# Kernel optimization log

Hardware: AMD Instinct MI355X
Metric: run time of the kernel (lower is better)

Reference implementation:

```python
import jax, jax.numpy as jnp
import numpy as np

LEAK = 0.95
THRESHOLD = 1.0
RESCALE = 2.0


def _xavier_uniform(key, shape, gain=2.0):
    fan_out, fan_in = shape
    bound = gain * np.sqrt(6.0 / (fan_in + fan_out))
    return jax.random.uniform(key, shape, jnp.float32, -bound, bound)


def setup_inputs() -> dict:
    key = jax.random.key(0)
    k_inp, k_w1, k_w2 = jax.random.split(key, 3)
    inp = jax.random.normal(k_inp, (8192, 784), jnp.float32)
    w1 = _xavier_uniform(k_w1, (800, 784))   # fc1.weight
    w2 = _xavier_uniform(k_w2, (10, 800))    # fc2.weight
    return {"inp": inp, "w1": w1, "w2": w2, "num_steps": 25}


@jax.custom_vjp
def spike_fn(x):
    return (x > 0).astype(x.dtype)

def _spike_fwd(x):
    return spike_fn(x), x

def _spike_bwd(x, g):
    # grad = g * 0.3 * relu(1 - |x|)  (surrogate BP)
    return (g * 0.3 * jnp.maximum(1.0 - jnp.abs(x), 0.0),)

spike_fn.defvjp(_spike_fwd, _spike_bwd)


def poisson_gen(key, inp):
    r = jax.random.uniform(key, inp.shape, inp.dtype)
    temp = (r * RESCALE <= jnp.abs(inp)).astype(inp.dtype) * jnp.sign(inp)
    return 0.5 * (temp + 1.0)


def reference(inp, w1, w2, num_steps):
    batch = inp.shape[0]
    x = inp.reshape(batch, -1)
    keys = jax.random.split(jax.random.key(42), num_steps)

    def step(carry, key):
        mem1, mem2 = carry
        sp = poisson_gen(key, x)                    # [B, 784]
        mem1 = LEAK * mem1 + (1.0 - LEAK) * (sp @ w1.T)  # [B, 800]
        mem_thr = mem1 / THRESHOLD - 1.0
        out = spike_fn(mem_thr)
        rst = jnp.where(mem_thr > 0, THRESHOLD, 0.0)
        mem1 = mem1 - jax.lax.stop_gradient(rst)
        mem2 = mem2 + out @ w2.T                    # [B, 10]
        return (mem1, mem2), None

    init = (jnp.zeros((batch, 800), x.dtype), jnp.zeros((batch, 10), x.dtype))
    (_, mem2), _ = jax.lax.scan(step, init, keys)
    return mem2 / num_steps
```

## Files before the change

### kernel.cpp

```cpp
#include <hip/hip_runtime.h>
#include <cstdint>

__host__ __device__ inline uint32_t tf_rotl32(uint32_t x, uint32_t r) {
  return (x << r) | (x >> (32u - r));
}

__host__ __device__ inline void threefry2x32(uint32_t k0, uint32_t k1,
                                             uint32_t x0, uint32_t x1,
                                             uint32_t* o0, uint32_t* o1) {
  uint32_t ks0 = k0, ks1 = k1, ks2 = k0 ^ k1 ^ 0x1BD11BDAu;
  x0 += ks0; x1 += ks1;
#define TF_R(r) { x0 += x1; x1 = tf_rotl32(x1, r); x1 ^= x0; }
  TF_R(13) TF_R(15) TF_R(26) TF_R(6)
  x0 += ks1; x1 += ks2 + 1u;
  TF_R(17) TF_R(29) TF_R(16) TF_R(24)
  x0 += ks2; x1 += ks0 + 2u;
  TF_R(13) TF_R(15) TF_R(26) TF_R(6)
  x0 += ks0; x1 += ks1 + 3u;
  TF_R(17) TF_R(29) TF_R(16) TF_R(24)
  x0 += ks1; x1 += ks2 + 4u;
  TF_R(13) TF_R(15) TF_R(26) TF_R(6)
  x0 += ks2; x1 += ks0 + 5u;
#undef TF_R
  *o0 = x0; *o1 = x1;
}

#define BSZ   8192
#define KIN   784
#define HID   800
#define NOUT  10
#define NSTEP 25


__global__ __launch_bounds__(256) void enc_kernel(const float* __restrict__ inp,
                                                  uint8_t* __restrict__ enc,
                                                  uint32_t k0, uint32_t k1) {
  int j = blockIdx.x * blockDim.x + threadIdx.x;
  if (j >= BSZ * KIN) return;
  uint32_t o0, o1;
  threefry2x32(k0, k1, 0u, (uint32_t)j, &o0, &o1);
  uint32_t bits = o0 ^ o1;
  float r = __uint_as_float((bits >> 9) | 0x3f800000u) - 1.0f;
  float x = inp[j];
  bool cond = (2.0f * r <= fabsf(x));
  int s = (x > 0.0f) ? 1 : ((x < 0.0f) ? -1 : 0);
  enc[j] = (uint8_t)(1 + (cond ? s : 0));
}

__global__ __launch_bounds__(256) void transpose_kernel(const float* __restrict__ w1,
                                                        float* __restrict__ w1t) {
  int idx = blockIdx.x * blockDim.x + threadIdx.x;
  if (idx >= KIN * HID) return;
  int k = idx / HID, n = idx % HID;
  w1t[idx] = w1[(size_t)n * KIN + k];
}

#define BM 256
#define BN 16
#define BK 16

typedef uint32_t u32;

__device__ __forceinline__ float cvt_ub(u32 x, int i) {
  return (float)((x >> (8 * i)) & 0xffu);
}

__global__ __launch_bounds__(256) void gemm_kernel(const uint8_t* __restrict__ enc,
                                                   const float* __restrict__ w1t,
                                                   float* __restrict__ gp) {
  const int panel  = blockIdx.z;
  const int kstart = panel * 264;
  const bool htail = (panel != 2);
  const int m0 = blockIdx.x * BM;
  const int n0 = blockIdx.y * BN;
  const int t  = threadIdx.x;
  const int lane = t & 63;
  const int wv   = t >> 6;

  const int r0 = wv * 64 + lane;
  const uint8_t* arow = enc + (size_t)(m0 + r0) * KIN + kstart;

  float acc[16];
#pragma unroll
  for (int c = 0; c < 16; c++) acc[c] = 0.0f;

  const int nld = htail ? 17 : 16;

  uint4 acur = *(const uint4*)(arow);
  uint4 anext;

  for (int tile = 0; tile < 16; tile++) {
    if (tile + 1 < nld)
      anext = *(const uint4*)(arow + (size_t)(tile + 1) * BK);
    const u32 w[4] = {acur.x, acur.y, acur.z, acur.w};
    const float* tb = w1t + (size_t)(kstart + tile * BK) * HID + n0;
#pragma unroll
    for (int kk = 0; kk < 16; kk++) {
      float a0 = cvt_ub(w[kk >> 2], kk & 3);
      const float* brow = tb + (size_t)kk * HID;
#pragma unroll
      for (int c = 0; c < 16; c++)
        acc[c] = __builtin_fmaf(a0, brow[c], acc[c]);
    }
    acur = anext;
  }
  if (htail) {
    const u32 w[2] = {acur.x, acur.y};
    const float* tb = w1t + (size_t)(kstart + 256) * HID + n0;
#pragma unroll
    for (int kk = 0; kk < 8; kk++) {
      float a0 = cvt_ub(w[kk >> 2], kk & 3);
      const float* brow = tb + (size_t)kk * HID;
#pragma unroll
      for (int c = 0; c < 16; c++)
        acc[c] = __builtin_fmaf(a0, brow[c], acc[c]);
    }
  }

  const size_t GS = (size_t)BSZ * HID;
  float* o0 = gp + (size_t)panel * GS + (size_t)(m0 + r0) * HID + n0;
#pragma unroll
  for (int c = 0; c < 16; c += 4) {
    float4 v0 = {acc[c], acc[c + 1], acc[c + 2], acc[c + 3]};
    *(float4*)(o0 + c) = v0;
  }
}

__global__ __launch_bounds__(256) void update_kernel(const float* __restrict__ gp,
                                                     float* __restrict__ mem1,
                                                     const float* __restrict__ w2,
                                                     float* __restrict__ mem2) {
  __shared__ float w2s[NOUT * HID];
  for (int i = threadIdx.x; i < NOUT * HID; i += 256) w2s[i] = w2[i];
  __syncthreads();

  const int wave = threadIdx.x / 64;
  const int lane = threadIdx.x % 64;
  const int b = blockIdx.x * 4 + wave;

  const size_t GS = (size_t)BSZ * HID;
  const float* g0 = gp + (size_t)b * HID;
  const float* g1 = g0 + GS;
  const float* g2 = g1 + GS;
  float* mrow = mem1 + (size_t)b * HID;

  float acc[NOUT];
#pragma unroll
  for (int i = 0; i < NOUT; i++) acc[i] = 0.0f;

  for (int j = lane; j < HID; j += 64) {
    float gs = __fmul_rn(0.5f, __fadd_rn(__fadd_rn(g0[j], g1[j]), g2[j]));
    float m = __fadd_rn(__fmul_rn(0.95f, mrow[j]), __fmul_rn(0.05f, gs));
    bool spike = __fadd_rn(m, -1.0f) > 0.0f;
    mrow[j] = spike ? __fadd_rn(m, -1.0f) : m;
    if (spike) {
#pragma unroll
      for (int i = 0; i < NOUT; i++) acc[i] += w2s[i * HID + j];
    }
  }
#pragma unroll
  for (int i = 0; i < NOUT; i++) {
    float v = acc[i];
    for (int off = 32; off > 0; off >>= 1) v += __shfl_down(v, off);
    if (lane == 0) mem2[(size_t)b * NOUT + i] += v;
  }
}

__global__ __launch_bounds__(256) void finalize_kernel(const float* __restrict__ mem2,
                                                       const int* __restrict__ ns,
                                                       float* __restrict__ out) {
  int i = blockIdx.x * blockDim.x + threadIdx.x;
  if (i < BSZ * NOUT) out[i] = mem2[i] / (float)(*ns);
}

extern "C" void kernel_launch(void* const* d_in, const int* in_sizes, int n_in,
                              void* d_out, int out_size, void* d_ws, size_t ws_size,
                              hipStream_t stream) {
  const float* inp = (const float*)d_in[0];
  const float* w1  = (const float*)d_in[1];
  const float* w2  = (const float*)d_in[2];
  const int*   dns = (const int*)d_in[3];
  float* out = (float*)d_out;

  char* ws = (char*)d_ws;
  size_t off = 0;
  uint8_t* enc = (uint8_t*)(ws + off);  off += (size_t)BSZ * KIN;
  off = (off + 255) & ~(size_t)255;
  float* w1t  = (float*)(ws + off);     off += (size_t)KIN * HID * 4;
  float* gp   = (float*)(ws + off);     off += (size_t)3 * BSZ * HID * 4;
  float* mem1 = (float*)(ws + off);     off += (size_t)BSZ * HID * 4;
  float* mem2 = (float*)(ws + off);     off += (size_t)BSZ * NOUT * 4;

  (void)hipMemsetAsync(mem1, 0, (size_t)BSZ * HID * 4, stream);
  (void)hipMemsetAsync(mem2, 0, (size_t)BSZ * NOUT * 4, stream);

  transpose_kernel<<<(KIN * HID + 255) / 256, 256, 0, stream>>>(w1, w1t);

  uint32_t keys[NSTEP][2];
  for (int t = 0; t < NSTEP; t++)
    threefry2x32(0u, 42u, 0u, (uint32_t)t, &keys[t][0], &keys[t][1]);

  const int n_elem = BSZ * KIN;
  for (int t = 0; t < NSTEP; t++) {
    enc_kernel<<<(n_elem + 255) / 256, 256, 0, stream>>>(inp, enc, keys[t][0], keys[t][1]);
    gemm_kernel<<<dim3(BSZ / BM, HID / BN, 3), 256, 0, stream>>>(enc, w1t, gp);
    update_kernel<<<BSZ / 4, 256, 0, stream>>>(gp, mem1, w2, mem2);
  }
  finalize_kernel<<<(BSZ * NOUT + 255) / 256, 256, 0, stream>>>(mem2, dns, out);
}
```

Measured before the change: 4.293 ms.

## Merge split-K GEMM panels in-kernel to drop partial-sum buffer traffic

The GEMM no longer splits K across three grid panels that each write a separate partial result. Each block now walks the full K range, combining the per-panel partial sums in registers with the same rounding order, and writes a single halved output. The update kernel then reads one buffer instead of three. This removes two extra 26MB writes and reads per step, at the cost of a third as many blocks with three times longer serial K loops, which reduces parallelism.

```diff
diff --git a/kernel.cpp b/kernel.cpp
--- a/kernel.cpp
+++ b/kernel.cpp
@@ -57,7 +57,6 @@
 
 #define BM 256
 #define BN 16
-#define BK 16
 
 typedef uint32_t u32;
 
@@ -67,66 +66,73 @@
 
 __global__ __launch_bounds__(256) void gemm_kernel(const uint8_t* __restrict__ enc,
                                                    const float* __restrict__ w1t,
-                                                   float* __restrict__ gp) {
-  const int panel  = blockIdx.z;
-  const int kstart = panel * 264;
-  const bool htail = (panel != 2);
+                                                   float* __restrict__ g) {
   const int m0 = blockIdx.x * BM;
   const int n0 = blockIdx.y * BN;
   const int t  = threadIdx.x;
-  const int lane = t & 63;
-  const int wv   = t >> 6;
-
-  const int r0 = wv * 64 + lane;
-  const uint8_t* arow = enc + (size_t)(m0 + r0) * KIN + kstart;
-
-  float acc[16];
+
+  const uint8_t* arow = enc + (size_t)(m0 + t) * KIN;
+
+  float acc[16], tot[16];
 #pragma unroll
   for (int c = 0; c < 16; c++) acc[c] = 0.0f;
 
-  const int nld = htail ? 17 : 16;
-
-  uint4 acur = *(const uint4*)(arow);
-  uint4 anext;
-
-  for (int tile = 0; tile < 16; tile++) {
-    if (tile + 1 < nld)
-      anext = *(const uint4*)(arow + (size_t)(tile + 1) * BK);
-    const u32 w[4] = {acur.x, acur.y, acur.z, acur.w};
-    const float* tb = w1t + (size_t)(kstart + tile * BK) * HID + n0;
-#pragma unroll
-    for (int kk = 0; kk < 16; kk++) {
+  auto run16 = [&](int ks) {
+    uint4 acur = *(const uint4*)(arow + ks);
+    for (int tile = 0; tile < 16; tile++) {
+      uint4 anext;
+      if (tile < 15)
+        anext = *(const uint4*)(arow + ks + (size_t)(tile + 1) * 16);
+      const u32 w[4] = {acur.x, acur.y, acur.z, acur.w};
+      const float* tb = w1t + (size_t)(ks + tile * 16) * HID + n0;
+#pragma unroll
+      for (int kk = 0; kk < 16; kk++) {
+        float a0 = cvt_ub(w[kk >> 2], kk & 3);
+        const float* brow = tb + (size_t)kk * HID;
+#pragma unroll
+        for (int c = 0; c < 16; c++)
+          acc[c] = __builtin_fmaf(a0, brow[c], acc[c]);
+      }
+      acur = anext;
+    }
+  };
+  auto run8 = [&](int ks) {
+    uint2 av = *(const uint2*)(arow + ks);
+    const u32 w[2] = {av.x, av.y};
+    const float* tb = w1t + (size_t)ks * HID + n0;
+#pragma unroll
+    for (int kk = 0; kk < 8; kk++) {
       float a0 = cvt_ub(w[kk >> 2], kk & 3);
       const float* brow = tb + (size_t)kk * HID;
 #pragma unroll
       for (int c = 0; c < 16; c++)
         acc[c] = __builtin_fmaf(a0, brow[c], acc[c]);
     }
-    acur = anext;
-  }
-  if (htail) {
-    const u32 w[2] = {acur.x, acur.y};
-    const float* tb = w1t + (size_t)(kstart + 256) * HID + n0;
-#pragma unroll
-    for (int kk = 0; kk < 8; kk++) {
-      float a0 = cvt_ub(w[kk >> 2], kk & 3);
-      const float* brow = tb + (size_t)kk * HID;
-#pragma unroll
-      for (int c = 0; c < 16; c++)
-        acc[c] = __builtin_fmaf(a0, brow[c], acc[c]);
-    }
-  }
-
-  const size_t GS = (size_t)BSZ * HID;
-  float* o0 = gp + (size_t)panel * GS + (size_t)(m0 + r0) * HID + n0;
+  };
+
+  run16(0);
+  run8(256);
+#pragma unroll
+  for (int c = 0; c < 16; c++) { tot[c] = acc[c]; acc[c] = 0.0f; }
+  run8(264);
+  run16(272);
+#pragma unroll
+  for (int c = 0; c < 16; c++) { tot[c] = __fadd_rn(tot[c], acc[c]); acc[c] = 0.0f; }
+  run16(528);
+
+  float* o0 = g + (size_t)(m0 + t) * HID + n0;
 #pragma unroll
   for (int c = 0; c < 16; c += 4) {
-    float4 v0 = {acc[c], acc[c + 1], acc[c + 2], acc[c + 3]};
+    float4 v0;
+    v0.x = __fmul_rn(0.5f, __fadd_rn(tot[c + 0], acc[c + 0]));
+    v0.y = __fmul_rn(0.5f, __fadd_rn(tot[c + 1], acc[c + 1]));
+    v0.z = __fmul_rn(0.5f, __fadd_rn(tot[c + 2], acc[c + 2]));
+    v0.w = __fmul_rn(0.5f, __fadd_rn(tot[c + 3], acc[c + 3]));
     *(float4*)(o0 + c) = v0;
   }
 }
 
-__global__ __launch_bounds__(256) void update_kernel(const float* __restrict__ gp,
+__global__ __launch_bounds__(256) void update_kernel(const float* __restrict__ g,
                                                      float* __restrict__ mem1,
                                                      const float* __restrict__ w2,
                                                      float* __restrict__ mem2) {
@@ -138,10 +144,7 @@
   const int lane = threadIdx.x % 64;
   const int b = blockIdx.x * 4 + wave;
 
-  const size_t GS = (size_t)BSZ * HID;
-  const float* g0 = gp + (size_t)b * HID;
-  const float* g1 = g0 + GS;
-  const float* g2 = g1 + GS;
+  const float* grow = g + (size_t)b * HID;
   float* mrow = mem1 + (size_t)b * HID;
 
   float acc[NOUT];
@@ -149,8 +152,7 @@
   for (int i = 0; i < NOUT; i++) acc[i] = 0.0f;
 
   for (int j = lane; j < HID; j += 64) {
-    float gs = __fmul_rn(0.5f, __fadd_rn(__fadd_rn(g0[j], g1[j]), g2[j]));
-    float m = __fadd_rn(__fmul_rn(0.95f, mrow[j]), __fmul_rn(0.05f, gs));
+    float m = __fadd_rn(__fmul_rn(0.95f, mrow[j]), __fmul_rn(0.05f, grow[j]));
     bool spike = __fadd_rn(m, -1.0f) > 0.0f;
     mrow[j] = spike ? __fadd_rn(m, -1.0f) : m;
     if (spike) {
@@ -187,7 +189,7 @@
   uint8_t* enc = (uint8_t*)(ws + off);  off += (size_t)BSZ * KIN;
   off = (off + 255) & ~(size_t)255;
   float* w1t  = (float*)(ws + off);     off += (size_t)KIN * HID * 4;
-  float* gp   = (float*)(ws + off);     off += (size_t)3 * BSZ * HID * 4;
+  float* g    = (float*)(ws + off);     off += (size_t)BSZ * HID * 4;
   float* mem1 = (float*)(ws + off);     off += (size_t)BSZ * HID * 4;
   float* mem2 = (float*)(ws + off);     off += (size_t)BSZ * NOUT * 4;
 
@@ -203,8 +205,8 @@
   const int n_elem = BSZ * KIN;
   for (int t = 0; t < NSTEP; t++) {
     enc_kernel<<<(n_elem + 255) / 256, 256, 0, stream>>>(inp, enc, keys[t][0], keys[t][1]);
-    gemm_kernel<<<dim3(BSZ / BM, HID / BN, 3), 256, 0, stream>>>(enc, w1t, gp);
-    update_kernel<<<BSZ / 4, 256, 0, stream>>>(gp, mem1, w2, mem2);
+    gemm_kernel<<<dim3(BSZ / BM, HID / BN), 256, 0, stream>>>(enc, w1t, g);
+    update_kernel<<<BSZ / 4, 256, 0, stream>>>(g, mem1, w2, mem2);
   }
   finalize_kernel<<<(BSZ * NOUT + 255) / 256, 256, 0, stream>>>(mem2, dns, out);
 }
```

New measurement: 5.196 ms. 1.21x slower.
